# Kernel tuning notes

Measured on AMD Instinct MI355X. Metric: run time of the kernel, lower is better.

## Reference

```python
import jax, jax.numpy as jnp
import numpy as np

D = 256          # node_embedding_dim (= GRU hidden per direction)
N = 1024         # number of frame nodes
C = 5            # num_classes
COUNTS = [15, 40, 15]   # num_intervals_per_scale
BINS = [80, 60, 80]     # dist_bins_list
MAX_T = 512      # fixed pad length for per-interval sequences (jit-static)


def _quant(w):
    # int8 per-tensor symmetric fake-quant with straight-through estimator
    s = jnp.maximum(jnp.max(jnp.abs(w)) / 127.0, 1e-8)
    q = jnp.clip(jnp.round(w / s), -128, 127) * s
    return w + jax.lax.stop_gradient(q - w)


def _gru_dir(x, eff, wih, whh, bih, bhh):
    # x: [I, T, D] packed-at-front sequences, eff: [I] valid lengths (>=1)
    # masked scan == torch packed GRU final hidden state
    I, T, _ = x.shape
    H = whh.shape[1]
    valid = jnp.arange(T)[None, :] < eff[:, None]   # [I, T]

    def step(h, inp):
        x_t, v = inp                                # [I,D], [I]
        gi = x_t @ wih.T + bih                      # [I, 3H]
        gh = h @ whh.T + bhh
        ir, iz, inn = jnp.split(gi, 3, axis=1)
        hr, hz, hn = jnp.split(gh, 3, axis=1)
        r = jax.nn.sigmoid(ir + hr)
        z = jax.nn.sigmoid(iz + hz)
        n = jnp.tanh(inn + r * hn)
        h = jnp.where(v[:, None], (1.0 - z) * n + z * h, h)
        return h, None

    h0 = jnp.zeros((I, H), x.dtype)
    hF, _ = jax.lax.scan(step, h0, (jnp.swapaxes(x, 0, 1), valid.T))
    return hF


def _forward(node_embeddings, time_positions, node_pred, audio_len, anchor_intervals,
             gru_wih, gru_whh, gru_bih, gru_bhh, w1, w2,
             w3_s0, w3_s1, w3_s2, sw_s0, ew_s0, sw_s1, ew_s1, sw_s2, ew_s2):
    al = audio_len[0]
    tpos = time_positions[:, 0] * al                     # [N]
    abn = jax.nn.softmax(node_pred, axis=-1)[:, 0]       # abnormal scores [N]
    w3s = [w3_s0, w3_s1, w3_s2]
    sws = [sw_s0, sw_s1, sw_s2]
    ews = [ew_s0, ew_s1, ew_s2]
    offs = np.concatenate([[0], np.cumsum(COUNTS)])
    bounds, confs, clss = [], [], []
    for si in range(3):
        I, b = COUNTS[si], BINS[si]
        anc = anchor_intervals[offs[si]:offs[si + 1]]    # [I, 2]
        starts, ends = anc[:, 0], anc[:, 1]
        # interval membership mask [I, N]
        mask = (tpos[None, :] >= starts[:, None]) & (tpos[None, :] <= ends[:, None])
        # compact valid nodes to the front (stable, preserves node order like x[mask])
        order = jnp.argsort(jnp.logical_not(mask), axis=1, stable=True)[:, :MAX_T]
        msort = jnp.take_along_axis(mask, order, axis=1)
        x_loc = node_embeddings[order] * msort[..., None]   # [I, MAX_T, D]; empty -> zeros row
        eff = jnp.clip(mask.sum(axis=1), 1, MAX_T)          # empty interval behaves as one zero step
        hf = _gru_dir(x_loc, eff, gru_wih[si, 0], gru_whh[si, 0], gru_bih[si, 0], gru_bhh[si, 0])
        # backward direction: reverse each valid prefix
        rev_idx = jnp.clip(eff[:, None] - 1 - jnp.arange(MAX_T)[None, :], 0, MAX_T - 1)
        x_rev = jnp.take_along_axis(x_loc, rev_idx[..., None], axis=1)
        hb = _gru_dir(x_rev, eff, gru_wih[si, 1], gru_whh[si, 1], gru_bih[si, 1], gru_bhh[si, 1])
        # shared feature: [2D | abnormal | center | width | 4 zero pads] = 2D+7
        feat = jnp.concatenate([
            hf, hb,
            abn[:I, None],
            ((starts + ends) * 0.5 / al)[:, None],
            ((ends - starts) / al)[:, None],
            jnp.zeros((I, 4), hf.dtype),
        ], axis=1)
        h = jax.nn.relu(feat @ _quant(w1[si]).T)   # dropout = identity (eval)
        h = jax.nn.relu(h @ _quant(w2[si]).T)
        out = h @ _quant(w3s[si]).T                # [I, 2b+1+(C-1)]
        so = jnp.sum(jax.nn.softmax(out[:, :b], axis=1) * sws[si], axis=1)
        eo = jnp.sum(jax.nn.softmax(out[:, b:2 * b], axis=1) * ews[si], axis=1)
        bounds.append(jnp.stack([jnp.clip(starts + so, 0.0, al), jnp.clip(ends + eo, 0.0, al)], axis=1))
        confs.append(out[:, 2 * b])
        clss.append(out[:, 2 * b + 1:])
    return (jnp.concatenate(bounds, axis=0),   # final_bounds [70, 2]
            jnp.concatenate(confs, axis=0),    # interval_conf_logits [70]
            jnp.concatenate(clss, axis=0))     # interval_cls_logits [70, 4]


def setup_inputs() -> dict:
    key = jax.random.key(0)
    ks = jax.random.split(key, 16)
    inp = {}
    inp["node_embeddings"] = jax.random.normal(ks[0], (N, D), jnp.float32)
    inp["time_positions"] = jax.random.uniform(ks[1], (N, 1), dtype=jnp.float32)
    inp["node_pred"] = jax.random.normal(ks[2], (N, C), jnp.float32)
    inp["audio_len"] = jnp.ones((1,), jnp.float32)
    rng = np.random.default_rng(0)
    widths = [0.05, 0.12, 0.30]
    rows = []
    for c, w in zip(COUNTS, widths):
        s = rng.uniform(0.0, 1.0 - w, size=c).astype(np.float32)
        e = s + rng.uniform(0.5 * w, w, size=c).astype(np.float32)
        rows.append(np.stack([s, e], axis=1))
    inp["anchor_intervals"] = jnp.asarray(np.concatenate(rows, axis=0))
    H = D
    def u(k, shape, fan):
        lim = 1.0 / np.sqrt(fan)
        return jax.random.uniform(k, shape, jnp.float32, -lim, lim)
    # GRU params stacked over [scale, direction]
    inp["gru_wih"] = u(ks[3], (3, 2, 3 * H, D), H)
    inp["gru_whh"] = u(ks[4], (3, 2, 3 * H, H), H)
    inp["gru_bih"] = u(ks[5], (3, 2, 3 * H), H)
    inp["gru_bhh"] = u(ks[6], (3, 2, 3 * H), H)
    F_in = 2 * D + 7
    inp["w1"] = u(ks[7], (3, 256, F_in), F_in)
    inp["w2"] = u(ks[8], (3, 256, 256), 256)
    inp["w3_s0"] = u(ks[9], (2 * BINS[0] + 1 + (C - 1), 256), 256)
    inp["w3_s1"] = u(ks[10], (2 * BINS[1] + 1 + (C - 1), 256), 256)
    inp["w3_s2"] = u(ks[11], (2 * BINS[2] + 1 + (C - 1), 256), 256)
    for i, nb in enumerate(BINS):
        inp[f"sw_s{i}"] = jnp.linspace(-20.0, 20.0, nb, dtype=jnp.float32)
        inp[f"ew_s{i}"] = jnp.linspace(-20.0, 20.0, nb, dtype=jnp.float32)
    return inp


def reference(node_embeddings, time_positions, node_pred, audio_len, anchor_intervals,
              gru_wih, gru_whh, gru_bih, gru_bhh, w1, w2,
              w3_s0, w3_s1, w3_s2, sw_s0, ew_s0, sw_s1, ew_s1, sw_s2, ew_s2):
    return _forward(node_embeddings, time_positions, node_pred, audio_len, anchor_intervals,
                    gru_wih, gru_whh, gru_bih, gru_bhh, w1, w2,
                    w3_s0, w3_s1, w3_s2, sw_s0, ew_s0, sw_s1, ew_s1, sw_s2, ew_s2)
```

## Files before the change

### kernel.cpp

```cpp
#include <hip/hip_runtime.h>
#include <math.h>

#define NN 1024
#define NNP 1025
#define DD 256
#define CC 5
#define G3 768
#define MAXT 512
#define NA 70
#define PW3 176

typedef _Float16 v4h __attribute__((ext_vector_type(4)));
typedef int v4i __attribute__((ext_vector_type(4)));

__device__ __forceinline__ int scale_of(int a){ return (a<15)?0:((a<55)?1:2); }
__device__ __forceinline__ int off_of(int s){ return (s==0)?0:((s==1)?15:55); }

__device__ __forceinline__ float sigf(float x){ return __fdividef(1.f, 1.f + __expf(-x)); }
__device__ __forceinline__ float tanhf_fast(float x){ return 1.f - __fdividef(2.f, __expf(2.f*x) + 1.f); }

__global__ void init_qs(unsigned int* __restrict__ qsb){
  if (threadIdx.x < 16) qsb[threadIdx.x] = 0u;
}

__global__ __launch_bounds__(256) void prep_kernel(
    const float* __restrict__ node_pred, const float* __restrict__ tp_in,
    const float* __restrict__ audio_len, const float* __restrict__ anchors,
    const float* __restrict__ whh,
    const float* __restrict__ bih, const float* __restrict__ bhh,
    const float* __restrict__ w1, const float* __restrict__ w2,
    const float* __restrict__ w30, const float* __restrict__ w31, const float* __restrict__ w32,
    float* __restrict__ abn, int* __restrict__ order, int* __restrict__ cnteff,
    unsigned int* __restrict__ qsb, float* __restrict__ cm, _Float16* __restrict__ E){
  int b = blockIdx.x, tid = threadIdx.x;
  if (b < 4){
    int i = b*256 + tid;
    float pv[CC]; float m = -1e30f;
    for (int c=0;c<CC;++c){ pv[c]=node_pred[i*CC+c]; m=fmaxf(m,pv[c]); }
    float s=0.f;
    for (int c=0;c<CC;++c) s += expf(pv[c]-m);
    abn[i] = expf(pv[0]-m)/s;
  } else if (b < 74){
    if (tid >= 64) return;
    int a = b-4; int lane = tid;
    float al = audio_len[0];
    float s = anchors[2*a], e = anchors[2*a+1];
    int* ord = order + a*MAXT;
    int cnt = 0;
    for (int base=0; base<NN; base+=64){
      float tp = tp_in[base+lane]*al;
      bool msk = (tp>=s)&&(tp<=e);
      unsigned long long bal = __ballot(msk);
      int off = (int)__popcll(bal & ((1ull<<lane)-1ull));
      if (msk && (cnt+off)<MAXT) ord[cnt+off] = base+lane;
      cnt += (int)__popcll(bal);
    }
    if (lane==0){ int c = cnt<MAXT?cnt:MAXT; cnteff[2*a]=c; cnteff[2*a+1]=(c>0)?c:1; }
  } else if (b < 218){
    int m = (b-74)>>4, s = (b-74)&15;
    const float* p; int n;
    if (m<3){ p = w1 + (size_t)m*256*519; n = 256*519; }
    else if (m<6){ p = w2 + (size_t)(m-3)*256*256; n = 256*256; }
    else { p = (m==6)?w30:((m==7)?w31:w32); n = ((m==7)?125:165)*256; }
    float mx = 0.f;
    for (int i = s*256+tid; i<n; i += 16*256) mx = fmaxf(mx, fabsf(p[i]));
    #pragma unroll
    for (int sh=1; sh<64; sh<<=1) mx = fmaxf(mx, __shfl_xor(mx, sh));
    if ((tid&63)==0) atomicMax(&qsb[m], __float_as_uint(mx));
  } else if (b < 1370){
    int row = (b-218)*4 + (tid>>6);
    int lane = tid&63;
    float4 v = reinterpret_cast<const float4*>(whh)[(size_t)row*64 + lane];
    float mx = fmaxf(fmaxf(fabsf(v.x),fabsf(v.y)), fmaxf(fabsf(v.z),fabsf(v.w)));
    #pragma unroll
    for (int sh=1; sh<64; sh<<=1) mx = fmaxf(mx, __shfl_xor(mx, sh));
    if (lane==0) cm[row] = fmaxf(mx, 1e-12f);
  } else {
    int i = (b-1370)*256 + tid;
    if (i >= 4608) return;
    int gt = i % 3; int c = (i/3)&255; int sd = i/768;
    int j = gt*256 + c;
    float v = bih[sd*G3+j] + ((gt<2)? bhh[sd*G3+j] : 0.f);
    E[((size_t)(sd*NNP + NN))*1024 + c*4 + gt] = (_Float16)v;
  }
}

__global__ __launch_bounds__(256) void quant_kernel(
    const float* __restrict__ whh, const float* __restrict__ cm,
    const float* __restrict__ w1, const float* __restrict__ w2,
    const float* __restrict__ w30, const float* __restrict__ w31, const float* __restrict__ w32,
    const unsigned int* __restrict__ qsb,
    uint4* __restrict__ whhB8, float* __restrict__ w1T, float* __restrict__ w2T, float* __restrict__ w3T){
  int b = blockIdx.x, tid = threadIdx.x;
  if (b < 288){
    int i = b*256 + tid;
    int q    = i & 3;
    int nt   = (i>>2) % 6;
    int lane = (i/24) & 63;
    int wv   = (i/1536) & 7;
    int sd   = i/12288;
    int gt = nt>>1, half = nt&1;
    int j = gt*256 + wv*32 + half*16 + (lane&15);
    int kbase = 64*q + 16*(lane>>4);
    float inv = 127.f/cm[sd*G3 + j];
    const float* src = whh + ((size_t)sd*G3 + j)*DD + kbase;
    unsigned int dw[4];
    #pragma unroll
    for (int d2=0; d2<4; ++d2){
      unsigned int acc = 0;
      #pragma unroll
      for (int e2=0; e2<4; ++e2){
        float qv = rintf(src[4*d2+e2]*inv);
        qv = fminf(fmaxf(qv,-127.f),127.f);
        int iq = (int)qv;
        acc |= ((unsigned int)(iq & 255)) << (8*e2);
      }
      dw[d2] = acc;
    }
    uint4 v; v.x=dw[0]; v.y=dw[1]; v.z=dw[2]; v.w=dw[3];
    whhB8[i] = v;
  } else if (b < 1056){
    int row = b-288; int si = row>>8; int j = row&255;
    float sc = fmaxf(__uint_as_float(qsb[si])/127.f, 1e-8f);
    const float* src = w1 + ((size_t)si*256 + j)*519;
    #pragma unroll
    for (int it=0; it<3; ++it){
      int k = it*256 + tid;
      if (k >= 520) break;
      float v = 0.f;
      if (k < 519){
        float q = rintf(src[k]/sc);
        q = fminf(fmaxf(q,-128.f),127.f);
        v = q*sc;
      }
      w1T[((size_t)si*520 + k)*256 + j] = v;
    }
  } else if (b < 1824){
    int row = b-1056; int si = row>>8; int j = row&255;
    float sc = fmaxf(__uint_as_float(qsb[3+si])/127.f, 1e-8f);
    const float* src = w2 + ((size_t)si*256 + j)*256;
    float q = rintf(src[tid]/sc);
    q = fminf(fmaxf(q,-128.f),127.f);
    w2T[((size_t)si*256 + tid)*256 + j] = q*sc;
  } else {
    int row = b-1824; int si = row/PW3; int j = row%PW3;
    int nout = (si==1)?125:165;
    const float* w3 = (si==0)?w30:((si==1)?w31:w32);
    float v = 0.f;
    if (j < nout){
      float sc = fmaxf(__uint_as_float(qsb[6+si])/127.f, 1e-8f);
      float q = rintf(w3[(size_t)j*256 + tid]/sc);
      q = fminf(fmaxf(q,-128.f),127.f);
      v = q*sc;
    }
    w3T[((size_t)si*256 + tid)*PW3 + j] = v;
  }
}

__global__ __launch_bounds__(256) void e_gemm(const float* __restrict__ emb, const float* __restrict__ wih,
                       const float* __restrict__ bih, const float* __restrict__ bhh,
                       _Float16* __restrict__ E){
  int sd = blockIdx.z;
  int row0 = blockIdx.x*64, col0 = blockIdx.y*64;
  const float* W = wih + (size_t)sd*G3*DD;
  __shared__ float As[64][65];
  __shared__ float Bs[64][65];
  int tid = threadIdx.x;
  int tr = tid>>4, tc = tid&15;
  float acc[4][4] = {};
  for (int kb=0; kb<4; ++kb){
    for (int i=0;i<4;++i){
      int e4 = i*256 + tid;
      int rr = e4>>4, qq = e4&15;
      float4 av = reinterpret_cast<const float4*>(emb)[ (size_t)(row0+rr)*64 + kb*16 + qq ];
      As[rr][qq*4+0]=av.x; As[rr][qq*4+1]=av.y; As[rr][qq*4+2]=av.z; As[rr][qq*4+3]=av.w;
      float4 bv = reinterpret_cast<const float4*>(W)[ (size_t)(col0+rr)*64 + kb*16 + qq ];
      Bs[rr][qq*4+0]=bv.x; Bs[rr][qq*4+1]=bv.y; Bs[rr][qq*4+2]=bv.z; Bs[rr][qq*4+3]=bv.w;
    }
    __syncthreads();
    for (int k=0;k<64;++k){
      float a0[4], b0[4];
      #pragma unroll
      for (int i=0;i<4;++i) a0[i]=As[tr*4+i][k];
      #pragma unroll
      for (int j=0;j<4;++j) b0[j]=Bs[tc*4+j][k];
      #pragma unroll
      for (int i=0;i<4;++i)
        #pragma unroll
        for (int j=0;j<4;++j)
          acc[i][j] += a0[i]*b0[j];
    }
    __syncthreads();
  }
  for (int i=0;i<4;++i){
    int row = row0 + tr*4 + i;
    for (int j=0;j<4;++j){
      int col = col0 + tc*4 + j;
      int gt = col>>8; int c = col&255;
      float val = acc[i][j] + bih[sd*G3+col] + ((gt<2)? bhh[sd*G3+col] : 0.f);
      E[((size_t)(sd*NNP + row))*1024 + c*4 + gt] = (_Float16)val;
    }
  }
}

__global__ __launch_bounds__(512, 2) void gru_kernel(
                           const _Float16* __restrict__ E, const v4i* __restrict__ whhB8,
                           const float* __restrict__ bhh, const float* __restrict__ cm,
                           const int* __restrict__ order, const int* __restrict__ cnteff,
                           float* __restrict__ hout){
  int a = blockIdx.x>>1, d = blockIdx.x&1;
  int si = scale_of(a);
  int sd = si*2+d;
  int tid = threadIdx.x;
  int w = tid>>6, lane = tid&63;
  int g16 = lane>>4;
  int ct = g16 & 1;

  __shared__ int ord_s[MAXT];
  __shared__ alignas(16) signed char h8[2][DD];

  ord_s[tid] = order[a*MAXT + tid];
  if (tid < DD) h8[0][tid] = 0;

  int cnt = cnteff[2*a], eff = cnteff[2*a+1];

  int c = w*32 + (lane&31);
  float bn = bhh[sd*G3 + 2*DD + c];
  const float ISQ = 1.f/(127.f*127.f);
  float sr = cm[sd*G3 +        c]*ISQ;
  float sz = cm[sd*G3 + 256 +  c]*ISQ;
  float sn = cm[sd*G3 + 512 +  c]*ISQ;

  v4i bf[6][4];
  {
    const v4i* wp = whhB8 + (((size_t)sd*8 + w)*64 + lane)*24;
    #pragma unroll
    for (int nt=0;nt<6;++nt)
      #pragma unroll
      for (int q=0;q<4;++q)
        bf[nt][q] = wp[nt*4+q];
  }

  const uint2* Eb = reinterpret_cast<const uint2*>(E) + (size_t)sd*NNP*256;

  float h = 0.f;
  uint2 gEven, gOdd;
  {
    int idx0 = d ? (eff-1) : 0;
    int n0 = (idx0 < cnt) ? ord_s[idx0] : NN;
    gEven = Eb[(size_t)n0*256 + c];
  }
  __syncthreads();

  for (int t=0;t<eff;++t){
    int p = t & 1;
    if (t+1 < eff){
      int idx1 = d ? (eff-2-t) : (t+1);
      int n1 = (idx1 < cnt) ? ord_s[idx1] : NN;
      if (p==0) gOdd  = Eb[(size_t)n1*256 + c];
      else      gEven = Eb[(size_t)n1*256 + c];
    }
    v4i acc0={0,0,0,0}, acc1={0,0,0,0}, acc2={0,0,0,0};
    v4i acc3={0,0,0,0}, acc4={0,0,0,0}, acc5={0,0,0,0};
    #pragma unroll
    for (int q=0;q<4;++q){
      v4i af = *reinterpret_cast<const v4i*>(&h8[p][64*q + 16*g16]);
      acc0 = __builtin_amdgcn_mfma_i32_16x16x64_i8(af, bf[0][q], acc0, 0,0,0);
      acc1 = __builtin_amdgcn_mfma_i32_16x16x64_i8(af, bf[1][q], acc1, 0,0,0);
      acc2 = __builtin_amdgcn_mfma_i32_16x16x64_i8(af, bf[2][q], acc2, 0,0,0);
      acc3 = __builtin_amdgcn_mfma_i32_16x16x64_i8(af, bf[3][q], acc3, 0,0,0);
      acc4 = __builtin_amdgcn_mfma_i32_16x16x64_i8(af, bf[4][q], acc4, 0,0,0);
      acc5 = __builtin_amdgcn_mfma_i32_16x16x64_i8(af, bf[5][q], acc5, 0,0,0);
    }
    v4h ev = __builtin_bit_cast(v4h, (p==0) ? gEven : gOdd);
    int ir  = (ct==0) ? acc0[0] : acc1[0];
    int iz  = (ct==0) ? acc2[0] : acc3[0];
    int inn = (ct==0) ? acc4[0] : acc5[0];
    float r  = sigf((float)ev[0] + (float)ir*sr);
    float z  = sigf((float)ev[1] + (float)iz*sz);
    float nv = tanhf_fast((float)ev[2] + r*((float)inn*sn + bn));
    h = z*(h - nv) + nv;
    if (lane < 32) h8[p^1][c] = (signed char)(int)rintf(h*127.f);
    __syncthreads();
  }
  if (lane < 32) hout[(size_t)(2*a+d)*DD + c] = h;
}

__global__ __launch_bounds__(256) void mlp_kernel(const float* __restrict__ hout, const float* __restrict__ abn,
                           const float* __restrict__ anchors, const float* __restrict__ audio_len,
                           const float* __restrict__ w1T, const float* __restrict__ w2T,
                           const float* __restrict__ w3T,
                           const float* __restrict__ sw0, const float* __restrict__ ew0,
                           const float* __restrict__ sw1, const float* __restrict__ ew1,
                           const float* __restrict__ sw2, const float* __restrict__ ew2,
                           float* __restrict__ out){
  int a = blockIdx.x, tid = threadIdx.x;
  int si = scale_of(a);
  int il = a - off_of(si);
  float s = anchors[2*a], e = anchors[2*a+1];
  float al = audio_len[0];
  __shared__ float feat[520];
  __shared__ float h1[256], h2[256], o[PW3];
  feat[tid]    = hout[(size_t)(2*a+0)*DD + tid];
  feat[DD+tid] = hout[(size_t)(2*a+1)*DD + tid];
  if (tid==0){
    feat[512]=abn[il];
    feat[513]=(s+e)*0.5f/al;
    feat[514]=(e-s)/al;
    feat[515]=0.f; feat[516]=0.f; feat[517]=0.f; feat[518]=0.f; feat[519]=0.f;
  }
  __syncthreads();
  {
    const float* p1 = w1T + (size_t)si*520*256 + tid;
    float acc=0.f;
    #pragma unroll 4
    for (int k=0;k<519;++k) acc += feat[k]*p1[(size_t)k*256];
    h1[tid]=fmaxf(acc,0.f);
  }
  __syncthreads();
  {
    const float* p2 = w2T + (size_t)si*256*256 + tid;
    float acc=0.f;
    #pragma unroll 4
    for (int k=0;k<256;++k) acc += h1[k]*p2[(size_t)k*256];
    h2[tid]=fmaxf(acc,0.f);
  }
  __syncthreads();
  if (tid<PW3){
    const float* p3 = w3T + (size_t)si*256*PW3 + tid;
    float acc=0.f;
    #pragma unroll 4
    for (int k=0;k<256;++k) acc += h2[k]*p3[(size_t)k*PW3];
    o[tid]=acc;
  }
  __syncthreads();
  if (tid==0){
    int b = (si==1)?60:80;
    const float* sw = (si==0)?sw0:((si==1)?sw1:sw2);
    const float* ew = (si==0)?ew0:((si==1)?ew1:ew2);
    float m=-1e30f; for (int i=0;i<b;++i) m=fmaxf(m,o[i]);
    float se=0.f, wsum=0.f;
    for (int i=0;i<b;++i){ float t=expf(o[i]-m); se+=t; wsum+=t*sw[i]; }
    float so = wsum/se;
    m=-1e30f; for (int i=0;i<b;++i) m=fmaxf(m,o[b+i]);
    se=0.f; wsum=0.f;
    for (int i=0;i<b;++i){ float t=expf(o[b+i]-m); se+=t; wsum+=t*ew[i]; }
    float eo = wsum/se;
    out[2*a]   = fminf(fmaxf(s+so,0.f),al);
    out[2*a+1] = fminf(fmaxf(e+eo,0.f),al);
    out[140+a] = o[2*b];
    for (int c2=0;c2<4;++c2) out[210+4*a+c2] = o[2*b+1+c2];
  }
}

extern "C" void kernel_launch(void* const* d_in, const int* in_sizes, int n_in,
                              void* d_out, int out_size, void* d_ws, size_t ws_size,
                              hipStream_t stream){
  const float* emb   = (const float*)d_in[0];
  const float* tpin  = (const float*)d_in[1];
  const float* npred = (const float*)d_in[2];
  const float* alen  = (const float*)d_in[3];
  const float* anch  = (const float*)d_in[4];
  const float* wih   = (const float*)d_in[5];
  const float* whh   = (const float*)d_in[6];
  const float* bih   = (const float*)d_in[7];
  const float* bhh   = (const float*)d_in[8];
  const float* w1    = (const float*)d_in[9];
  const float* w2    = (const float*)d_in[10];
  const float* w30   = (const float*)d_in[11];
  const float* w31   = (const float*)d_in[12];
  const float* w32   = (const float*)d_in[13];
  const float* sw0   = (const float*)d_in[14];
  const float* ew0   = (const float*)d_in[15];
  const float* sw1   = (const float*)d_in[16];
  const float* ew1   = (const float*)d_in[17];
  const float* sw2   = (const float*)d_in[18];
  const float* ew2   = (const float*)d_in[19];

  char* ws = (char*)d_ws;
  size_t off = 0;
  auto take = [&](size_t bytes)->char*{
    char* p = ws + off;
    off = (off + bytes + 255) & ~(size_t)255;
    return p;
  };
  float* abn    = (float*)take((size_t)NN*4);
  int*   order_ = (int*)  take((size_t)NA*MAXT*4);
  int*   cnteff = (int*)  take((size_t)NA*2*4);
  unsigned int* qsb = (unsigned int*)take(16*4);
  float* cm     = (float*)take((size_t)6*G3*4);
  v4i*   whhB8  = (v4i*)  take((size_t)6*8*64*24*16);
  _Float16* E   = (_Float16*)take((size_t)6*NNP*1024*2);
  float* hout   = (float*)take((size_t)NA*2*DD*4);
  float* w1T    = (float*)take((size_t)3*520*256*4);
  float* w2T    = (float*)take((size_t)3*256*256*4);
  float* w3T    = (float*)take((size_t)3*256*PW3*4);
  (void)ws_size; (void)in_sizes; (void)n_in; (void)out_size;

  init_qs<<<dim3(1), dim3(64), 0, stream>>>(qsb);
  prep_kernel<<<dim3(1388), dim3(256), 0, stream>>>(npred, tpin, alen, anch, whh, bih, bhh,
                                                    w1, w2, w30, w31, w32,
                                                    abn, order_, cnteff, qsb, cm, E);
  e_gemm<<<dim3(16,12,6), dim3(256), 0, stream>>>(emb, wih, bih, bhh, E);
  quant_kernel<<<dim3(2352), dim3(256), 0, stream>>>(whh, cm, w1, w2, w30, w31, w32, qsb,
                                                     (uint4*)whhB8, w1T, w2T, w3T);
  gru_kernel<<<dim3(NA*2), dim3(512), 0, stream>>>(E, whhB8, bhh, cm, order_, cnteff, hout);
  mlp_kernel<<<dim3(NA), dim3(256), 0, stream>>>(hout, abn, anch, alen, w1T, w2T, w3T,
                                                 sw0, ew0, sw1, ew1, sw2, ew2, (float*)d_out);
}
```

Baseline: 462.4 us.

## Compute input-projection GEMM with fp16 MFMA on pre-packed operands

Replaces the fp32 shared-memory tiled GEMM for the GRU input projection with one 16x16x32 fp16 MFMA tile per wave. The embeddings and wih are pre-converted to fp16, and wih is pre-packed into the MFMA B-fragment layout inside prep_kernel. The weight abs-max reduction now uses one block per tensor with a shared-memory reduction instead of atomics, which removes the separate init launch. In exchange, the input projection runs on fp16 inputs, and the max reductions get less parallelism.

```diff
diff --git a/kernel.cpp b/kernel.cpp
--- a/kernel.cpp
+++ b/kernel.cpp
@@ -10,7 +10,9 @@
 #define NA 70
 #define PW3 176
 
+typedef _Float16 v8h __attribute__((ext_vector_type(8)));
 typedef _Float16 v4h __attribute__((ext_vector_type(4)));
+typedef float v4f __attribute__((ext_vector_type(4)));
 typedef int v4i __attribute__((ext_vector_type(4)));
 
 __device__ __forceinline__ int scale_of(int a){ return (a<15)?0:((a<55)?1:2); }
@@ -18,20 +20,18 @@
 
 __device__ __forceinline__ float sigf(float x){ return __fdividef(1.f, 1.f + __expf(-x)); }
 __device__ __forceinline__ float tanhf_fast(float x){ return 1.f - __fdividef(2.f, __expf(2.f*x) + 1.f); }
-
-__global__ void init_qs(unsigned int* __restrict__ qsb){
-  if (threadIdx.x < 16) qsb[threadIdx.x] = 0u;
-}
 
 __global__ __launch_bounds__(256) void prep_kernel(
     const float* __restrict__ node_pred, const float* __restrict__ tp_in,
     const float* __restrict__ audio_len, const float* __restrict__ anchors,
-    const float* __restrict__ whh,
+    const float* __restrict__ whh, const float* __restrict__ wih,
+    const float* __restrict__ emb,
     const float* __restrict__ bih, const float* __restrict__ bhh,
     const float* __restrict__ w1, const float* __restrict__ w2,
     const float* __restrict__ w30, const float* __restrict__ w31, const float* __restrict__ w32,
     float* __restrict__ abn, int* __restrict__ order, int* __restrict__ cnteff,
-    unsigned int* __restrict__ qsb, float* __restrict__ cm, _Float16* __restrict__ E){
+    float* __restrict__ qs, float* __restrict__ cm, _Float16* __restrict__ E,
+    _Float16* __restrict__ emb16, v8h* __restrict__ wihB){
   int b = blockIdx.x, tid = threadIdx.x;
   if (b < 4){
     int i = b*256 + tid;
@@ -56,32 +56,51 @@
       cnt += (int)__popcll(bal);
     }
     if (lane==0){ int c = cnt<MAXT?cnt:MAXT; cnteff[2*a]=c; cnteff[2*a+1]=(c>0)?c:1; }
-  } else if (b < 218){
-    int m = (b-74)>>4, s = (b-74)&15;
+  } else if (b < 83){
+    int m = b-74;
     const float* p; int n;
     if (m<3){ p = w1 + (size_t)m*256*519; n = 256*519; }
     else if (m<6){ p = w2 + (size_t)(m-3)*256*256; n = 256*256; }
     else { p = (m==6)?w30:((m==7)?w31:w32); n = ((m==7)?125:165)*256; }
     float mx = 0.f;
-    for (int i = s*256+tid; i<n; i += 16*256) mx = fmaxf(mx, fabsf(p[i]));
-    #pragma unroll
-    for (int sh=1; sh<64; sh<<=1) mx = fmaxf(mx, __shfl_xor(mx, sh));
-    if ((tid&63)==0) atomicMax(&qsb[m], __float_as_uint(mx));
-  } else if (b < 1370){
-    int row = (b-218)*4 + (tid>>6);
+    for (int i=tid;i<n;i+=256) mx = fmaxf(mx, fabsf(p[i]));
+    __shared__ float red[256];
+    red[tid]=mx; __syncthreads();
+    for (int sft=128; sft>0; sft>>=1){ if (tid<sft) red[tid]=fmaxf(red[tid],red[tid+sft]); __syncthreads(); }
+    if (tid==0) qs[m] = fmaxf(red[0]/127.f, 1e-8f);
+  } else if (b < 1235){
+    int row = (b-83)*4 + (tid>>6);
     int lane = tid&63;
     float4 v = reinterpret_cast<const float4*>(whh)[(size_t)row*64 + lane];
     float mx = fmaxf(fmaxf(fabsf(v.x),fabsf(v.y)), fmaxf(fabsf(v.z),fabsf(v.w)));
     #pragma unroll
     for (int sh=1; sh<64; sh<<=1) mx = fmaxf(mx, __shfl_xor(mx, sh));
     if (lane==0) cm[row] = fmaxf(mx, 1e-12f);
-  } else {
-    int i = (b-1370)*256 + tid;
+  } else if (b < 1253){
+    int i = (b-1235)*256 + tid;
     if (i >= 4608) return;
     int gt = i % 3; int c = (i/3)&255; int sd = i/768;
     int j = gt*256 + c;
     float v = bih[sd*G3+j] + ((gt<2)? bhh[sd*G3+j] : 0.f);
     E[((size_t)(sd*NNP + NN))*1024 + c*4 + gt] = (_Float16)v;
+  } else if (b < 1509){
+    int i = (b-1253)*256 + tid;
+    float4 v = reinterpret_cast<const float4*>(emb)[i];
+    v4h o; o[0]=(_Float16)v.x; o[1]=(_Float16)v.y; o[2]=(_Float16)v.z; o[3]=(_Float16)v.w;
+    *reinterpret_cast<v4h*>(emb16 + (size_t)i*4) = o;
+  } else {
+    int i = (b-1509)*256 + tid;
+    int q    = i & 7;
+    int lane = (i>>3) & 63;
+    int ct   = (i>>9) % 48;
+    int sd   = i / 24576;
+    int j = ct*16 + (lane&15);
+    int k0 = 32*q + 8*(lane>>4);
+    const float* src = wih + ((size_t)sd*G3 + j)*DD + k0;
+    v8h o;
+    #pragma unroll
+    for (int e2=0;e2<8;++e2) o[e2] = (_Float16)src[e2];
+    wihB[i] = o;
   }
 }
 
@@ -89,7 +108,7 @@
     const float* __restrict__ whh, const float* __restrict__ cm,
     const float* __restrict__ w1, const float* __restrict__ w2,
     const float* __restrict__ w30, const float* __restrict__ w31, const float* __restrict__ w32,
-    const unsigned int* __restrict__ qsb,
+    const float* __restrict__ qs,
     uint4* __restrict__ whhB8, float* __restrict__ w1T, float* __restrict__ w2T, float* __restrict__ w3T){
   int b = blockIdx.x, tid = threadIdx.x;
   if (b < 288){
@@ -121,7 +140,7 @@
     whhB8[i] = v;
   } else if (b < 1056){
     int row = b-288; int si = row>>8; int j = row&255;
-    float sc = fmaxf(__uint_as_float(qsb[si])/127.f, 1e-8f);
+    float sc = qs[si];
     const float* src = w1 + ((size_t)si*256 + j)*519;
     #pragma unroll
     for (int it=0; it<3; ++it){
@@ -137,7 +156,7 @@
     }
   } else if (b < 1824){
     int row = b-1056; int si = row>>8; int j = row&255;
-    float sc = fmaxf(__uint_as_float(qsb[3+si])/127.f, 1e-8f);
+    float sc = qs[3+si];
     const float* src = w2 + ((size_t)si*256 + j)*256;
     float q = rintf(src[tid]/sc);
     q = fminf(fmaxf(q,-128.f),127.f);
@@ -148,7 +167,7 @@
     const float* w3 = (si==0)?w30:((si==1)?w31:w32);
     float v = 0.f;
     if (j < nout){
-      float sc = fmaxf(__uint_as_float(qsb[6+si])/127.f, 1e-8f);
+      float sc = qs[6+si];
       float q = rintf(w3[(size_t)j*256 + tid]/sc);
       q = fminf(fmaxf(q,-128.f),127.f);
       v = q*sc;
@@ -157,49 +176,33 @@
   }
 }
 
-__global__ __launch_bounds__(256) void e_gemm(const float* __restrict__ emb, const float* __restrict__ wih,
+__global__ __launch_bounds__(256) void e_gemm(const _Float16* __restrict__ emb16,
+                       const v8h* __restrict__ wihB,
                        const float* __restrict__ bih, const float* __restrict__ bhh,
                        _Float16* __restrict__ E){
   int sd = blockIdx.z;
-  int row0 = blockIdx.x*64, col0 = blockIdx.y*64;
-  const float* W = wih + (size_t)sd*G3*DD;
-  __shared__ float As[64][65];
-  __shared__ float Bs[64][65];
   int tid = threadIdx.x;
-  int tr = tid>>4, tc = tid&15;
-  float acc[4][4] = {};
-  for (int kb=0; kb<4; ++kb){
-    for (int i=0;i<4;++i){
-      int e4 = i*256 + tid;
-      int rr = e4>>4, qq = e4&15;
-      float4 av = reinterpret_cast<const float4*>(emb)[ (size_t)(row0+rr)*64 + kb*16 + qq ];
-      As[rr][qq*4+0]=av.x; As[rr][qq*4+1]=av.y; As[rr][qq*4+2]=av.z; As[rr][qq*4+3]=av.w;
-      float4 bv = reinterpret_cast<const float4*>(W)[ (size_t)(col0+rr)*64 + kb*16 + qq ];
-      Bs[rr][qq*4+0]=bv.x; Bs[rr][qq*4+1]=bv.y; Bs[rr][qq*4+2]=bv.z; Bs[rr][qq*4+3]=bv.w;
-    }
-    __syncthreads();
-    for (int k=0;k<64;++k){
-      float a0[4], b0[4];
-      #pragma unroll
-      for (int i=0;i<4;++i) a0[i]=As[tr*4+i][k];
-      #pragma unroll
-      for (int j=0;j<4;++j) b0[j]=Bs[tc*4+j][k];
-      #pragma unroll
-      for (int i=0;i<4;++i)
-        #pragma unroll
-        for (int j=0;j<4;++j)
-          acc[i][j] += a0[i]*b0[j];
-    }
-    __syncthreads();
-  }
-  for (int i=0;i<4;++i){
-    int row = row0 + tr*4 + i;
-    for (int j=0;j<4;++j){
-      int col = col0 + tc*4 + j;
-      int gt = col>>8; int c = col&255;
-      float val = acc[i][j] + bih[sd*G3+col] + ((gt<2)? bhh[sd*G3+col] : 0.f);
-      E[((size_t)(sd*NNP + row))*1024 + c*4 + gt] = (_Float16)val;
-    }
+  int w = tid>>6, lane = tid&63;
+  int tile = blockIdx.x*4 + w;
+  int r_t = tile & 63, c_t = tile >> 6;
+  int row0 = r_t*16, col0 = c_t*16;
+  int j = col0 + (lane&15);
+  float bsum = bih[sd*G3 + j] + (((j>>8) < 2) ? bhh[sd*G3 + j] : 0.f);
+
+  const _Float16* A = emb16 + (size_t)(row0 + (lane&15))*DD + 8*(lane>>4);
+  const v8h* B = wihB + (((size_t)sd*48 + c_t)*64 + lane)*8;
+
+  v4f acc = {0.f,0.f,0.f,0.f};
+  #pragma unroll
+  for (int q=0;q<8;++q){
+    v8h af = *reinterpret_cast<const v8h*>(A + 32*q);
+    acc = __builtin_amdgcn_mfma_f32_16x16x32_f16(af, B[q], acc, 0,0,0);
+  }
+  int gt = j>>8, c = j&255;
+  #pragma unroll
+  for (int r=0;r<4;++r){
+    int row = row0 + (lane>>4)*4 + r;
+    E[((size_t)(sd*NNP + row))*1024 + c*4 + gt] = (_Float16)(acc[r] + bsum);
   }
 }
 
@@ -387,7 +390,7 @@
   float* abn    = (float*)take((size_t)NN*4);
   int*   order_ = (int*)  take((size_t)NA*MAXT*4);
   int*   cnteff = (int*)  take((size_t)NA*2*4);
-  unsigned int* qsb = (unsigned int*)take(16*4);
+  float* qs     = (float*)take(16*4);
   float* cm     = (float*)take((size_t)6*G3*4);
   v4i*   whhB8  = (v4i*)  take((size_t)6*8*64*24*16);
   _Float16* E   = (_Float16*)take((size_t)6*NNP*1024*2);
@@ -395,14 +398,15 @@
   float* w1T    = (float*)take((size_t)3*520*256*4);
   float* w2T    = (float*)take((size_t)3*256*256*4);
   float* w3T    = (float*)take((size_t)3*256*PW3*4);
+  _Float16* emb16 = (_Float16*)take((size_t)NN*DD*2);
+  v8h*   wihB   = (v8h*)take((size_t)6*48*64*8*16);
   (void)ws_size; (void)in_sizes; (void)n_in; (void)out_size;
 
-  init_qs<<<dim3(1), dim3(64), 0, stream>>>(qsb);
-  prep_kernel<<<dim3(1388), dim3(256), 0, stream>>>(npred, tpin, alen, anch, whh, bih, bhh,
-                                                    w1, w2, w30, w31, w32,
-                                                    abn, order_, cnteff, qsb, cm, E);
-  e_gemm<<<dim3(16,12,6), dim3(256), 0, stream>>>(emb, wih, bih, bhh, E);
-  quant_kernel<<<dim3(2352), dim3(256), 0, stream>>>(whh, cm, w1, w2, w30, w31, w32, qsb,
+  prep_kernel<<<dim3(2085), dim3(256), 0, stream>>>(npred, tpin, alen, anch, whh, wih, emb,
+                                                    bih, bhh, w1, w2, w30, w31, w32,
+                                                    abn, order_, cnteff, qs, cm, E, emb16, wihB);
+  e_gemm<<<dim3(768,1,6), dim3(256), 0, stream>>>(emb16, wihB, bih, bhh, E);
+  quant_kernel<<<dim3(2352), dim3(256), 0, stream>>>(whh, cm, w1, w2, w30, w31, w32, qs,
                                                      (uint4*)whhB8, w1T, w2T, w3T);
   gru_kernel<<<dim3(NA*2), dim3(512), 0, stream>>>(E, whhB8, bhh, cm, order_, cnteff, hout);
   mlp_kernel<<<dim3(NA), dim3(256), 0, stream>>>(hout, abn, anch, alen, w1T, w2T, w3T,
```

Result: slower. 508.4 us (+10.0%).
